# Optimization experiments

Measured on AMD Instinct MI355X. Metric: run time of the kernel, lower is better.

The kernel has to match this reference:

```python
import jax, jax.numpy as jnp
import numpy as np

B, SRC_SEQ, SRC_DIMS = 1024, 336, 64
ORDER, TAR_SEQ = 168, 96


def setup_inputs() -> dict:
    key = jax.random.key(0)
    k1, k2 = jax.random.split(key, 2)
    inputs = jax.random.normal(k1, (B, SRC_SEQ, SRC_DIMS), dtype=jnp.float32)
    # Per-channel Dense(order -> tar_seq_len): stacked kernels and biases.
    W = jax.random.normal(k2, (SRC_DIMS, ORDER, TAR_SEQ), dtype=jnp.float32) * (1.0 / np.sqrt(ORDER))
    b = jnp.zeros((SRC_DIMS, TAR_SEQ), dtype=jnp.float32)
    return {"inputs": inputs, "W": W, "b": b, "training": 0}


def reference(inputs, W, b, training):
    # inputs: [B, S, C]; W: [C, order, T]; b: [C, T]
    order = W.shape[1]
    x = jnp.transpose(inputs, (0, 2, 1))[:, :, -order:]  # [B, C, order]
    # Fused per-channel linear projection (batched over channels):
    y = jnp.einsum('bco,cot->bct', x, W) + b             # [B, C, T]
    return jnp.transpose(y, (0, 2, 1))                    # [B, T, C]
```

## Files before the change

kernel.cpp:

```cpp
#include <hip/hip_runtime.h>

#define BATCH 1024
#define SEQ   336
#define CCH   64
#define ORD   168
#define TT    96
#define OFF   168
#define KP    192
#define NKC   6
#define NCHK  24
#define RSC   25

typedef __attribute__((ext_vector_type(8))) short  short8;
typedef __attribute__((ext_vector_type(8))) unsigned short ushort8;
typedef __attribute__((ext_vector_type(4))) float  floatx4;

#define WT2_ELEMS ((size_t)CCH * 36 * 512)
#define WS_NEED   (WT2_ELEMS * 2)

__device__ __forceinline__ unsigned short f2bf(float f) {
    union { float f; unsigned u; } v; v.f = f;
    unsigned r = v.u + 0x7FFF + ((v.u >> 16) & 1);
    return (unsigned short)(r >> 16);
}

__global__ __launch_bounds__(256)
void k1w(const float* __restrict__ W, unsigned short* __restrict__ Wt2)
{
    const int tid = threadIdx.x, l = tid & 63, w = tid >> 6;
    const int wid = blockIdx.x * 4 + w;
    const int kc = wid % 6;
    const int n  = (wid / 6) % 6;
    const int c  = wid / 36;
    const int m  = l & 15, kg = l >> 4;
    const int t  = n * 16 + m;
    ushort8 u;
    #pragma unroll
    for (int j = 0; j < 8; ++j) {
        int o = kc * 32 + kg * 8 + j;
        float val = (o < ORD) ? W[((size_t)c * ORD + o) * TT + t] : 0.f;
        u[j] = f2bf(val);
    }
    *(ushort8*)(Wt2 + (size_t)wid * 512 + l * 8) = u;
}

__global__ __launch_bounds__(256, 2)
void k2f(const float* __restrict__ inp, const unsigned short* __restrict__ Wt2,
         const float* __restrict__ bias, float* __restrict__ out)
{
    __shared__ unsigned short Xs[8 * 16 * RSC * 8];

    const int tid = threadIdx.x, l = tid & 63, wv = tid >> 6;
    const int m = l & 15, kg = l >> 4;
    const int btile = (blockIdx.x & 7) | ((blockIdx.x >> 6) << 3);
    const int cg    = (blockIdx.x >> 3) & 7;
    const int b0 = btile * 16, c0 = cg * 8;

    #pragma unroll
    for (int i = 0; i < 3; ++i) {
        int v = tid + i * 256;
        int cq = v & 1, b = (v >> 1) & 15, kchunk = v >> 5;
        floatx4 f[8];
        #pragma unroll
        for (int j = 0; j < 8; ++j) {
            int o = kchunk * 8 + j;
            floatx4 z = {0.f, 0.f, 0.f, 0.f};
            f[j] = (o < ORD)
                ? *(const floatx4*)(inp + ((size_t)(b0 + b) * SEQ + OFF + o) * CCH + c0 + cq * 4)
                : z;
        }
        #pragma unroll
        for (int cc = 0; cc < 4; ++cc) {
            int c = cq * 4 + cc;
            ushort8 u;
            #pragma unroll
            for (int j = 0; j < 8; ++j) u[j] = f2bf(f[j][cc]);
            *(ushort8*)(Xs + (((c * 16 + b) * RSC + (kchunk ^ (c & 7))) << 3)) = u;
        }
    }

    float bv[2][6];
    #pragma unroll
    for (int cc = 0; cc < 2; ++cc)
        #pragma unroll
        for (int n = 0; n < 6; ++n)
            bv[cc][n] = bias[(c0 + wv * 2 + cc) * TT + n * 16 + m];

    __syncthreads();

    floatx4 acc[2][6] = {};
    #pragma unroll
    for (int cc = 0; cc < 2; ++cc) {
        const int c = wv * 2 + cc;
        short8 a[6];
        #pragma unroll
        for (int kc = 0; kc < 6; ++kc) {
            int chunk = (kc * 4 + kg) ^ (c & 7);
            a[kc] = *(const short8*)(Xs + (((c * 16 + m) * RSC + chunk) << 3));
        }
        const unsigned short* Wc = Wt2 + (size_t)(c0 + c) * 36 * 512;
        #pragma unroll
        for (int kc = 0; kc < 6; ++kc) {
            #pragma unroll
            for (int n = 0; n < 6; ++n) {
                short8 bfrag = *(const short8*)(Wc + (size_t)(n * 6 + kc) * 512 + l * 8);
                acc[cc][n] = __builtin_amdgcn_mfma_f32_16x16x32_bf16(a[kc], bfrag, acc[cc][n], 0, 0, 0);
            }
        }
    }

    __syncthreads();

    float* Ys = (float*)Xs;
    #pragma unroll
    for (int n = 0; n < 6; ++n) {
        #pragma unroll
        for (int cc = 0; cc < 2; ++cc) {
            int c = wv * 2 + cc;
            #pragma unroll
            for (int r = 0; r < 4; ++r) {
                int row = kg * 4 + r;
                Ys[row * 196 + m * 12 + c] = acc[cc][n][r] + bv[cc][n];
            }
        }
        __syncthreads();
        {
            int c4 = tid & 1, t = (tid >> 1) & 15, r8 = tid >> 5;
            #pragma unroll
            for (int rep = 0; rep < 2; ++rep) {
                int row = rep * 8 + r8;
                floatx4 y = *(const floatx4*)(Ys + row * 196 + t * 12 + c4 * 4);
                *(floatx4*)(out + ((size_t)(b0 + row) * TT + n * 16 + t) * CCH + c0 + c4 * 4) = y;
            }
        }
        __syncthreads();
    }
}

#define MB  8
#define NT  16
#define KO  8
#define NCH (ORD/KO)
#define WSTRIDE 132
typedef __attribute__((address_space(3))) void* lds_ptr_t;
typedef const __attribute__((address_space(1))) void* gbl_ptr_t;

__global__ __launch_bounds__(256, 4)
void tcl_fallback(const float* __restrict__ inp, const float* __restrict__ W,
                  const float* __restrict__ bias, float* __restrict__ out)
{
    __shared__ float Xsf[MB * KO * CCH];
    __shared__ float Wsf[CCH * WSTRIDE];
    const int tid = threadIdx.x;
    const int c   = tid & 63;
    const int tg  = tid >> 6;
    const int bblk = blockIdx.x & 127;
    const int tblk = blockIdx.x >> 7;
    const int b0 = bblk * MB;
    const int t0 = tblk * NT;
    float acc[MB][4];
    #pragma unroll
    for (int bi = 0; bi < MB; ++bi)
        #pragma unroll
        for (int tj = 0; tj < 4; ++tj) acc[bi][tj] = 0.f;
    for (int ch = 0; ch < NCH; ++ch) {
        const int ob = ch * KO;
        #pragma unroll
        for (int k = 0; k < 4; ++k) {
            int v = tid + k * 256;
            int row = v >> 4, c4 = v & 15;
            int bi = row >> 3, oi = row & 7;
            const float* gp = inp + ((size_t)(b0 + bi) * SEQ + (OFF + ob + oi)) * CCH + c4 * 4;
            __builtin_amdgcn_global_load_lds((gbl_ptr_t)gp, (lds_ptr_t)(Xsf + v * 4), 16, 0, 0);
        }
        float4 wbuf[8];
        #pragma unroll
        for (int k = 0; k < 8; ++k) {
            int v = tid + k * 256;
            int cch = v >> 5, oi = (v >> 2) & 7, t4 = v & 3;
            wbuf[k] = *(const float4*)(W + (size_t)cch * (ORD * TT) + (size_t)(ob + oi) * TT + t0 + t4 * 4);
        }
        #pragma unroll
        for (int k = 0; k < 8; ++k) {
            int v = tid + k * 256;
            int cch = v >> 5, oi = (v >> 2) & 7, t4 = v & 3;
            *(float4*)(Wsf + cch * WSTRIDE + oi * NT + t4 * 4) = wbuf[k];
        }
        __syncthreads();
        #pragma unroll
        for (int oi = 0; oi < KO; ++oi) {
            const float4 wvv = *(const float4*)(Wsf + c * WSTRIDE + oi * NT + tg * 4);
            float xv[MB];
            #pragma unroll
            for (int bi = 0; bi < MB; ++bi) xv[bi] = Xsf[(bi * KO + oi) * CCH + c];
            #pragma unroll
            for (int bi = 0; bi < MB; ++bi) {
                acc[bi][0] += xv[bi] * wvv.x;
                acc[bi][1] += xv[bi] * wvv.y;
                acc[bi][2] += xv[bi] * wvv.z;
                acc[bi][3] += xv[bi] * wvv.w;
            }
        }
        __syncthreads();
    }
    const float4 bvv = *(const float4*)(bias + c * TT + t0 + tg * 4);
    #pragma unroll
    for (int bi = 0; bi < MB; ++bi) {
        size_t base = ((size_t)(b0 + bi) * TT + (t0 + tg * 4)) * CCH + c;
        out[base]           = acc[bi][0] + bvv.x;
        out[base + CCH]     = acc[bi][1] + bvv.y;
        out[base + 2 * CCH] = acc[bi][2] + bvv.z;
        out[base + 3 * CCH] = acc[bi][3] + bvv.w;
    }
}

extern "C" void kernel_launch(void* const* d_in, const int* in_sizes, int n_in,
                              void* d_out, int out_size, void* d_ws, size_t ws_size,
                              hipStream_t stream) {
    const float* inp  = (const float*)d_in[0];
    const float* W    = (const float*)d_in[1];
    const float* bias = (const float*)d_in[2];
    float* out = (float*)d_out;

    if (ws_size >= WS_NEED) {
        unsigned short* Wt2 = (unsigned short*)d_ws;
        k1w<<<576, 256, 0, stream>>>(W, Wt2);
        k2f<<<512, 256, 0, stream>>>(inp, Wt2, bias, out);
    } else {
        tcl_fallback<<<768, 256, 0, stream>>>(inp, W, bias, out);
    }
}
```

Baseline: 146.8 us.

## Use 512-thread blocks with one channel per wave and single-pass epilogue

The main GEMM kernel moves from 256 to 512 threads per block, so each of the eight waves handles one channel instead of two. The input staging loads are issued for both iterations before conversion to raise memory-level parallelism. The output epilogue now stages all 96 target columns in a larger shared-memory buffer (about 55KB) and writes them in one pass, dropping the per-column-group barriers. The larger LDS footprint and launch bound may limit occupancy.

```diff
diff --git a/kernel.cpp b/kernel.cpp
--- a/kernel.cpp
+++ b/kernel.cpp
@@ -7,9 +7,8 @@
 #define TT    96
 #define OFF   168
 #define KP    192
-#define NKC   6
-#define NCHK  24
 #define RSC   25
+#define YSTR  9
 
 typedef __attribute__((ext_vector_type(8))) short  short8;
 typedef __attribute__((ext_vector_type(8))) unsigned short ushort8;
@@ -44,11 +43,12 @@
     *(ushort8*)(Wt2 + (size_t)wid * 512 + l * 8) = u;
 }
 
-__global__ __launch_bounds__(256, 2)
+__global__ __launch_bounds__(512, 4)
 void k2f(const float* __restrict__ inp, const unsigned short* __restrict__ Wt2,
          const float* __restrict__ bias, float* __restrict__ out)
 {
-    __shared__ unsigned short Xs[8 * 16 * RSC * 8];
+    __shared__ float smem_f[16 * TT * YSTR];
+    unsigned short* Xs = (unsigned short*)smem_f;
 
     const int tid = threadIdx.x, l = tid & 63, wv = tid >> 6;
     const int m = l & 15, kg = l >> 4;
@@ -56,42 +56,48 @@
     const int cg    = (blockIdx.x >> 3) & 7;
     const int b0 = btile * 16, c0 = cg * 8;
 
-    #pragma unroll
-    for (int i = 0; i < 3; ++i) {
-        int v = tid + i * 256;
-        int cq = v & 1, b = (v >> 1) & 15, kchunk = v >> 5;
-        floatx4 f[8];
-        #pragma unroll
-        for (int j = 0; j < 8; ++j) {
-            int o = kchunk * 8 + j;
-            floatx4 z = {0.f, 0.f, 0.f, 0.f};
-            f[j] = (o < ORD)
-                ? *(const floatx4*)(inp + ((size_t)(b0 + b) * SEQ + OFF + o) * CCH + c0 + cq * 4)
-                : z;
-        }
-        #pragma unroll
-        for (int cc = 0; cc < 4; ++cc) {
-            int c = cq * 4 + cc;
-            ushort8 u;
-            #pragma unroll
-            for (int j = 0; j < 8; ++j) u[j] = f2bf(f[j][cc]);
-            *(ushort8*)(Xs + (((c * 16 + b) * RSC + (kchunk ^ (c & 7))) << 3)) = u;
-        }
-    }
-
-    float bv[2][6];
-    #pragma unroll
-    for (int cc = 0; cc < 2; ++cc)
-        #pragma unroll
-        for (int n = 0; n < 6; ++n)
-            bv[cc][n] = bias[(c0 + wv * 2 + cc) * TT + n * 16 + m];
+    floatx4 f[2][8];
+    #pragma unroll
+    for (int i = 0; i < 2; ++i) {
+        int v = tid + i * 512;
+        if (v < 768) {
+            int cq = v & 1, b = (v >> 1) & 15, kchunk = v >> 5;
+            #pragma unroll
+            for (int j = 0; j < 8; ++j) {
+                int o = kchunk * 8 + j;
+                floatx4 z = {0.f, 0.f, 0.f, 0.f};
+                f[i][j] = (o < ORD)
+                    ? *(const floatx4*)(inp + ((size_t)(b0 + b) * SEQ + OFF + o) * CCH + c0 + cq * 4)
+                    : z;
+            }
+        }
+    }
+    #pragma unroll
+    for (int i = 0; i < 2; ++i) {
+        int v = tid + i * 512;
+        if (v < 768) {
+            int cq = v & 1, b = (v >> 1) & 15, kchunk = v >> 5;
+            #pragma unroll
+            for (int cc = 0; cc < 4; ++cc) {
+                int c = cq * 4 + cc;
+                ushort8 u;
+                #pragma unroll
+                for (int j = 0; j < 8; ++j) u[j] = f2bf(f[i][j][cc]);
+                *(ushort8*)(Xs + (((c * 16 + b) * RSC + (kchunk ^ (c & 7))) << 3)) = u;
+            }
+        }
+    }
+
+    float bv[6];
+    #pragma unroll
+    for (int n = 0; n < 6; ++n)
+        bv[n] = bias[(c0 + wv) * TT + n * 16 + m];
 
     __syncthreads();
 
-    floatx4 acc[2][6] = {};
-    #pragma unroll
-    for (int cc = 0; cc < 2; ++cc) {
-        const int c = wv * 2 + cc;
+    floatx4 acc[6] = {};
+    {
+        const int c = wv;
         short8 a[6];
         #pragma unroll
         for (int kc = 0; kc < 6; ++kc) {
@@ -104,36 +110,35 @@
             #pragma unroll
             for (int n = 0; n < 6; ++n) {
                 short8 bfrag = *(const short8*)(Wc + (size_t)(n * 6 + kc) * 512 + l * 8);
-                acc[cc][n] = __builtin_amdgcn_mfma_f32_16x16x32_bf16(a[kc], bfrag, acc[cc][n], 0, 0, 0);
+                acc[n] = __builtin_amdgcn_mfma_f32_16x16x32_bf16(a[kc], bfrag, acc[n], 0, 0, 0);
             }
         }
     }
 
     __syncthreads();
 
-    float* Ys = (float*)Xs;
-    #pragma unroll
-    for (int n = 0; n < 6; ++n) {
-        #pragma unroll
-        for (int cc = 0; cc < 2; ++cc) {
-            int c = wv * 2 + cc;
+    float* Ys = smem_f;
+    {
+        const int c = wv;
+        #pragma unroll
+        for (int n = 0; n < 6; ++n)
             #pragma unroll
             for (int r = 0; r < 4; ++r) {
                 int row = kg * 4 + r;
-                Ys[row * 196 + m * 12 + c] = acc[cc][n][r] + bv[cc][n];
-            }
-        }
-        __syncthreads();
-        {
-            int c4 = tid & 1, t = (tid >> 1) & 15, r8 = tid >> 5;
-            #pragma unroll
-            for (int rep = 0; rep < 2; ++rep) {
-                int row = rep * 8 + r8;
-                floatx4 y = *(const floatx4*)(Ys + row * 196 + t * 12 + c4 * 4);
-                *(floatx4*)(out + ((size_t)(b0 + row) * TT + n * 16 + t) * CCH + c0 + c4 * 4) = y;
-            }
-        }
-        __syncthreads();
+                Ys[(row * TT + n * 16 + m) * YSTR + c] = acc[n][r] + bv[n];
+            }
+    }
+    __syncthreads();
+    {
+        int c4  = tid & 1;
+        int te  = (tid >> 1) & 15;
+        int row = tid >> 5;
+        #pragma unroll
+        for (int s = 0; s < 6; ++s) {
+            int tt = te + s * 16;
+            floatx4 y = *(const floatx4*)(Ys + (row * TT + tt) * YSTR + c4 * 4);
+            *(floatx4*)(out + ((size_t)(b0 + row) * TT + tt) * CCH + c0 + c4 * 4) = y;
+        }
     }
 }
 
@@ -225,7 +230,7 @@
     if (ws_size >= WS_NEED) {
         unsigned short* Wt2 = (unsigned short*)d_ws;
         k1w<<<576, 256, 0, stream>>>(W, Wt2);
-        k2f<<<512, 256, 0, stream>>>(inp, Wt2, bias, out);
+        k2f<<<512, 512, 0, stream>>>(inp, Wt2, bias, out);
     } else {
         tcl_fallback<<<768, 256, 0, stream>>>(inp, W, bias, out);
     }
```

Result: no change. 146.7 us (-0.0%).
